# Kernel tuning notes

Measured on AMD Instinct MI355X. Metric: run time of the kernel, lower is better.

The kernel has to match this reference:

```python
import jax, jax.numpy as jnp
import numpy as np
import math

B, H, N, L = 8, 512, 64, 2048


def setup_inputs() -> dict:
    key = jax.random.key(0)
    k_u, k_c, k_dt, k_d, k_w, k_b, k_ar, k_ai = jax.random.split(key, 8)
    u = jax.random.normal(k_u, (B, H, L), dtype=jnp.float32)
    # C ~ complex randn, stored as (..., 2) real/imag pairs (torch.view_as_real)
    C_ri = jax.random.normal(k_c, (H, N, 2), dtype=jnp.float32)
    # log_dt ~ Uniform(log(dt_min), log(dt_max))
    lo, hi = math.log(0.001), math.log(0.1)
    log_dt = jax.random.uniform(k_dt, (H,), dtype=jnp.float32) * (hi - lo) + lo
    D = jax.random.normal(k_d, (H,), dtype=jnp.float32)
    # Conv1d(H, 2H, kernel_size=1) -> weight (2H, H), bias (2H), kaiming-ish scale
    W = jax.random.normal(k_w, (2 * H, H), dtype=jnp.float32) / math.sqrt(H)
    b = jax.random.normal(k_b, (2 * H,), dtype=jnp.float32) * 0.01
    # Fixed diagonal state matrix A: Re(A) uniform in [-0.9, -0.8), Im(A) random
    a_re = -0.9 + 0.1 * jax.random.uniform(k_ar, (N,), dtype=jnp.float32)
    a_im = math.pi * jnp.arange(N, dtype=jnp.float32)  # stable oscillation freqs
    A_ri = jnp.stack([a_re, a_im], axis=-1)
    return {"u": u, "C_ri": C_ri, "log_dt": log_dt, "D": D, "W": W, "b": b, "A_ri": A_ri}


def _forward(u, C_ri, log_dt, D, W, b, A_ri):
    Lseq = u.shape[-1]
    C = C_ri[..., 0] + 1j * C_ri[..., 1]          # (H, N) complex
    A = A_ri[..., 0] + 1j * A_ri[..., 1]          # (N,) complex
    dt = jnp.exp(log_dt)                           # (H,)
    dtA = dt[:, None] * A[None, :]                 # (H, N)
    # Vandermonde: exp(dtA * l) for l in [0, L)  -> (H, N, L) complex
    K = jnp.exp(dtA[:, :, None] * jnp.arange(Lseq, dtype=jnp.float32))
    Ct = C * (jnp.exp(dtA) - 1.0) / A              # (H, N)
    k = 2.0 * jnp.einsum('hn,hnl->hl', Ct, K).real  # (H, L) real kernel
    # FFT long convolution (linear conv via length-2L circular conv)
    nfft = 2 * Lseq
    y = jnp.fft.irfft(jnp.fft.rfft(u, n=nfft) * jnp.fft.rfft(k, n=nfft), n=nfft)[..., :Lseq]
    y = y + D[:, None] * u                         # skip connection
    y = jax.nn.gelu(y, approximate=False)          # torch nn.GELU default = exact erf
    # Conv1d kernel_size=1 == per-position linear, then GLU over channel dim
    z = jnp.einsum('oh,bhl->bol', W, y) + b[:, None]  # (B, 2H, L)
    a, g = jnp.split(z, 2, axis=-2)
    return a * jax.nn.sigmoid(g)                   # (B, H, L)


def reference(u, C_ri, log_dt, D, W, b, A_ri):
    return _forward(u, C_ri, log_dt, D, W, b, A_ri)
```

## Files before the change

kernel.cpp:

```cpp
#include <hip/hip_runtime.h>
#include <math.h>

#define Hh 512
#define Nn 64
#define Ll 2048
#define Bb 8

typedef float f32x4 __attribute__((ext_vector_type(4)));
typedef __bf16 bf16x8 __attribute__((ext_vector_type(8)));

__device__ __forceinline__ unsigned short f2b(float x) {
  unsigned u = __builtin_bit_cast(unsigned, x);
  u += 0x7FFFu + ((u >> 16) & 1u);
  return (unsigned short)(u >> 16);
}
__device__ __forceinline__ float b2f(unsigned short b) {
  unsigned u = ((unsigned)b) << 16;
  return __builtin_bit_cast(float, u);
}

union BF8 {
  unsigned short us[8];
  bf16x8 v;
  uint4 q;
};

__device__ __forceinline__ uint4 cvt8q(const float* p) {
  float4 a = *(const float4*)p;
  float4 b = *(const float4*)(p + 4);
  BF8 o;
  o.us[0] = f2b(a.x); o.us[1] = f2b(a.y); o.us[2] = f2b(a.z); o.us[3] = f2b(a.w);
  o.us[4] = f2b(b.x); o.us[5] = f2b(b.y); o.us[6] = f2b(b.z); o.us[7] = f2b(b.w);
  return o.q;
}

__device__ __forceinline__ float gelu_f(float y) {
  float t = y * y;
  float p = y * fmaf(0.0713548162726f, t, 1.59576912161f);
  float e = __expf(-p);
  return y / (1.0f + e);
}

__global__ __launch_bounds__(256) void prep_kernel(
    const float* __restrict__ C_ri, const float* __restrict__ log_dt,
    const float* __restrict__ A_ri, unsigned short* __restrict__ A1,
    unsigned short* __restrict__ A2, float* __restrict__ lamQ) {
  __shared__ char sm[49152];
  __shared__ float kqs[64];
  __shared__ float kpart[4][64];
  float* kt = (float*)sm;
  char* A1s = sm;
  char* A2s = sm + 16384;
  int h = blockIdx.x;
  int tid = threadIdx.x, n = tid & 63, part = tid >> 6;

  float dt = expf(log_dt[h]);
  float ar = A_ri[2 * n], ai = A_ri[2 * n + 1];
  float er = expf(dt * ar);
  float sn, cs;
  sincosf(dt * ai, &sn, &cs);
  float lr = er * cs, li = er * sn;
  float em1r = lr - 1.0f, em1i = li;
  float cr = C_ri[(h * 64 + n) * 2], ci = C_ri[(h * 64 + n) * 2 + 1];
  float numr = cr * em1r - ci * em1i;
  float numi = cr * em1i + ci * em1r;
  float den = ar * ar + ai * ai;
  float ctr = (numr * ar + numi * ai) / den;
  float cti = (numi * ar - numr * ai) / den;
  float l16r = lr, l16i = li;
#pragma unroll
  for (int s = 0; s < 4; ++s) {
    float t = l16r * l16r - l16i * l16i;
    l16i = 2.0f * l16r * l16i;
    l16r = t;
  }
  if (part == 0) {
    float qr = l16r, qi = l16i;
#pragma unroll
    for (int s = 0; s < 2; ++s) {
      float t = qr * qr - qi * qi;
      qi = 2.0f * qr * qi;
      qr = t;
    }
    lamQ[h * 128 + 2 * n] = qr;
    lamQ[h * 128 + 2 * n + 1] = qi;
  }
  float lpr = 1.0f, lpi = 0.0f;
  for (int s = 0; s < part; ++s) {
    float t = lpr * l16r - lpi * l16i;
    lpi = lpr * l16i + lpi * l16r;
    lpr = t;
  }
  int e0 = part * 16;
  {
    float vr = ctr * lpr - cti * lpi, vi = ctr * lpi + cti * lpr;
#pragma unroll
    for (int j = 0; j < 16; ++j) {
      kt[(e0 + j) * 64 + n] = vr;
      float t = vr * lr - vi * li;
      vi = vr * li + vi * lr;
      vr = t;
    }
  }
  __syncthreads();
  {
    float s = 0.0f;
#pragma unroll
    for (int j = 0; j < 16; ++j) s += kt[n * 64 + ((e0 + j + n) & 63)];
    kpart[part][n] = s;
  }
  __syncthreads();
  if (part == 0) kqs[n] = 2.0f * (kpart[0][n] + kpart[1][n] + kpart[2][n] + kpart[3][n]);
  __syncthreads();
  {
    BF8 R0, R1, I0, I1;
    float vr = lpr, vi = lpi;
#pragma unroll
    for (int j = 0; j < 16; ++j) {
      int idx = 15 - j;
      if (idx < 8) { R0.us[idx] = f2b(vr); I0.us[idx] = f2b(vi); }
      else         { R1.us[idx - 8] = f2b(vr); I1.us[idx - 8] = f2b(vi); }
      float t = vr * lr - vi * li;
      vi = vr * li + vi * lr;
      vr = t;
    }
    int qlo = 48 - e0;
    int rowR = 2 * n, rowI = 2 * n + 1;
    *(uint4*)(A1s + ((rowR * 128 + 2 * qlo) ^ ((rowR & 7) << 4))) = R0.q;
    *(uint4*)(A1s + ((rowR * 128 + 2 * qlo + 16) ^ ((rowR & 7) << 4))) = R1.q;
    *(uint4*)(A1s + ((rowI * 128 + 2 * qlo) ^ ((rowI & 7) << 4))) = I0.q;
    *(uint4*)(A1s + ((rowI * 128 + 2 * qlo + 16) ^ ((rowI & 7) << 4))) = I1.q;
  }
  {
    float c1r = ctr * lr - cti * li, c1i = ctr * li + cti * lr;
    float wr = 2.0f * (c1r * lpr - c1i * lpi);
    float wi = 2.0f * (c1r * lpi + c1i * lpr);
#pragma unroll
    for (int j = 0; j < 16; ++j) {
      int t = e0 + j;
      *(unsigned*)(A2s + ((t * 512 + 128 + 4 * n) ^ ((t & 7) << 4))) =
          (unsigned)f2b(wr) | ((unsigned)f2b(-wi) << 16);
      float tm = wr * lr - wi * li;
      wi = wr * li + wi * lr;
      wr = tm;
    }
  }
  {
    int tau = n;
#pragma unroll
    for (int half = 0; half < 2; ++half) {
      int q0 = e0 + half * 8;
      BF8 o;
#pragma unroll
      for (int j = 0; j < 8; ++j) {
        int q = q0 + j;
        o.us[j] = (q <= tau) ? f2b(kqs[tau - q]) : (unsigned short)0;
      }
      *(uint4*)(A2s + ((tau * 512 + 2 * q0) ^ ((tau & 7) << 4))) = o.q;
    }
  }
  __syncthreads();
#pragma unroll
  for (int i = 0; i < 4; ++i) {
    int byte = (i * 256 + tid) * 16;
    int row = byte >> 7;
    *(uint4*)((char*)A1 + (size_t)h * 16384 + byte) =
        *(const uint4*)(A1s + (byte ^ ((row & 7) << 4)));
  }
#pragma unroll
  for (int i = 0; i < 8; ++i) {
    int idx = i * 256 + tid;
    int row = idx >> 5;
    int byte = row * 512 + (idx & 31) * 16;
    *(uint4*)((char*)A2 + (size_t)h * 32768 + byte) =
        *(const uint4*)(A2s + (byte ^ ((row & 7) << 4)));
  }
}

__global__ __launch_bounds__(256) void wcvt_kernel(const float* __restrict__ W,
                                                   unsigned short* __restrict__ Wimg) {
  int id = blockIdx.x * 256 + threadIdx.x;
  int slot = id & 3, row = (id >> 2) & 127, kt = (id >> 9) & 15, ot = id >> 13;
  int o = (row < 64) ? (ot * 64 + row) : (512 + ot * 64 + row - 64);
  uint4 v = cvt8q(W + (size_t)o * 512 + kt * 32 + slot * 8);
  int sp = slot ^ ((row >> 1) & 3);
  *(uint4*)((char*)Wimg + (((size_t)ot * 16 + kt) * 8192) + row * 64 + sp * 16) = v;
}

__global__ __launch_bounds__(256, 5) void fused_conv_kernel(
    const float* __restrict__ u, const unsigned short* __restrict__ A1,
    const unsigned short* __restrict__ A2, const float* __restrict__ lamQ,
    const float* __restrict__ Dv, unsigned short* __restrict__ gy) {
  __shared__ char SXb[16384];
  __shared__ char Ub[8192];
  __shared__ float2 sX16[2][64];
  int h = blockIdx.x;
  int bs = blockIdx.y * 2;
  int tid = threadIdx.x;
  int w = tid >> 6, lane = tid & 63, lg = lane >> 4, l15 = lane & 15;

  {
    int row = tid >> 2, k0 = (tid & 3) * 16;
    int b = bs + (row >> 5), c = row & 31;
    const float* up = u + ((size_t)(b * Hh + h)) * Ll + c * 64 + k0;
    uint4 v0 = cvt8q(up), v1 = cvt8q(up + 8);
    int base = row * 128 + k0 * 2;
    int swz = (row & 7) << 4;
    *(uint4*)(Ub + (base ^ swz)) = v0;
    *(uint4*)(Ub + ((base + 16) ^ swz)) = v1;
  }
  bf16x8 a1f[2][2];
#pragma unroll
  for (int i = 0; i < 2; ++i) {
    int row = (2 * w + i) * 16 + l15;
#pragma unroll
    for (int kb = 0; kb < 2; ++kb)
      a1f[i][kb] = *(const bf16x8*)(A1 + ((size_t)h * 128 + row) * 64 + kb * 32 + lg * 8);
  }
  __syncthreads();

#pragma unroll
  for (int ct = 0; ct < 4; ++ct) {
    int bc = ct * 16 + l15;
    bf16x8 bu[2];
#pragma unroll
    for (int kb = 0; kb < 2; ++kb)
      bu[kb] = *(const bf16x8*)(Ub + ((bc * 128 + kb * 64 + lg * 16) ^ ((bc & 7) << 4)));
#pragma unroll
    for (int i = 0; i < 2; ++i) {
      f32x4 acc = {0.f, 0.f, 0.f, 0.f};
      acc = __builtin_amdgcn_mfma_f32_16x16x32_bf16(a1f[i][0], bu[0], acc, 0, 0, 0);
      acc = __builtin_amdgcn_mfma_f32_16x16x32_bf16(a1f[i][1], bu[1], acc, 0, 0, 0);
      int n2q = (2 * w + i) * 16 + lg * 4;
      uint2 pk;
      pk.x = f2b(acc[0]) | ((unsigned)f2b(acc[1]) << 16);
      pk.y = f2b(acc[2]) | ((unsigned)f2b(acc[3]) << 16);
      *(uint2*)(SXb + ((bc * 256 + n2q * 2) ^ ((bc & 7) << 4))) = pk;
    }
  }
  __syncthreads();

  bf16x8 a2f[6];
  int rowA = w * 16 + l15;
#pragma unroll
  for (int kb = 0; kb < 6; ++kb)
    a2f[kb] = *(const bf16x8*)(A2 + ((size_t)h * 64 + rowA) * 256 + kb * 32 + lg * 8);

  int nn = tid & 63, bpart = tid >> 6;
  int rbloc = bpart >> 1, rhalf = bpart & 1;
  float lqr = lamQ[h * 128 + 2 * nn], lqi = lamQ[h * 128 + 2 * nn + 1];
  {
    float Xr = 0.f, Xi = 0.f;
    int cbase = rbloc * 32 + rhalf * 16;
    for (int c = 0; c < 16; ++c) {
      int bc = cbase + c;
      int byte = (bc * 256 + 4 * nn) ^ ((bc & 7) << 4);
      unsigned ps = *(const unsigned*)(SXb + byte);
      *(unsigned*)(SXb + byte) = (unsigned)f2b(Xr) | ((unsigned)f2b(Xi) << 16);
      float Sr = b2f((unsigned short)(ps & 0xFFFF));
      float Si = b2f((unsigned short)(ps >> 16));
      float nXr = lqr * Xr - lqi * Xi + Sr;
      float nXi = lqr * Xi + lqi * Xr + Si;
      Xr = nXr;
      Xi = nXi;
    }
    if (rhalf == 0) sX16[rbloc][nn] = make_float2(Xr, Xi);
  }
  __syncthreads();
  if (rhalf) {
    float2 x16 = sX16[rbloc][nn];
    float cr = x16.x, ci = x16.y;
    int cbase = rbloc * 32 + 16;
#pragma unroll
    for (int c = 0; c < 16; ++c) {
      int bc = cbase + c;
      int byte = (bc * 256 + 4 * nn) ^ ((bc & 7) << 4);
      unsigned pv = *(const unsigned*)(SXb + byte);
      float vr = b2f((unsigned short)(pv & 0xFFFF)) + cr;
      float vi = b2f((unsigned short)(pv >> 16)) + ci;
      *(unsigned*)(SXb + byte) = (unsigned)f2b(vr) | ((unsigned)f2b(vi) << 16);
      float t = cr * lqr - ci * lqi;
      ci = cr * lqi + ci * lqr;
      cr = t;
    }
  }
  __syncthreads();

  float Dh = Dv[h];
  int t0 = w * 16 + lg * 4;
  f32x4 acc4[4];
  uint2 usk[4];
#pragma unroll
  for (int ct = 0; ct < 4; ++ct) {
    int bc = ct * 16 + l15;
    f32x4 acc = {0.f, 0.f, 0.f, 0.f};
#pragma unroll
    for (int kb = 0; kb < 2; ++kb) {
      bf16x8 bu = *(const bf16x8*)(Ub + ((bc * 128 + kb * 64 + lg * 16) ^ ((bc & 7) << 4)));
      acc = __builtin_amdgcn_mfma_f32_16x16x32_bf16(a2f[kb], bu, acc, 0, 0, 0);
    }
#pragma unroll
    for (int kb = 2; kb < 6; ++kb) {
      bf16x8 bx = *(const bf16x8*)(SXb + ((bc * 256 + ((kb - 2) * 32 + lg * 8) * 2) ^ ((bc & 7) << 4)));
      acc = __builtin_amdgcn_mfma_f32_16x16x32_bf16(a2f[kb], bx, acc, 0, 0, 0);
    }
    acc4[ct] = acc;
    usk[ct] = *(const uint2*)(Ub + ((bc * 128 + t0 * 2) ^ ((bc & 7) << 4)));
  }
  __syncthreads();

#pragma unroll
  for (int ct = 0; ct < 4; ++ct) {
    int bc = ct * 16 + l15;
    const unsigned short* up = (const unsigned short*)&usk[ct];
    unsigned short e[4];
#pragma unroll
    for (int r = 0; r < 4; ++r) {
      float y = fmaf(Dh, b2f(up[r]), acc4[ct][r]);
      e[r] = f2b(gelu_f(y));
    }
    uint2 pk;
    pk.x = e[0] | ((unsigned)e[1] << 16);
    pk.y = e[2] | ((unsigned)e[3] << 16);
    *(uint2*)(Ub + ((bc * 128 + t0 * 2) ^ ((bc & 7) << 4))) = pk;
  }
  __syncthreads();

#pragma unroll
  for (int i = 0; i < 2; ++i) {
    int j = tid + 256 * i;
    int row = j >> 3, q = j & 7;
    int byte = row * 128 + q * 16;
    uint4 v = *(const uint4*)(Ub + (byte ^ ((row & 7) << 4)));
    int b = bs + (row >> 5), c = row & 31;
    *(uint4*)(gy + ((size_t)(b * Hh + h)) * Ll + c * 64 + q * 8) = v;
  }
}

__global__ __launch_bounds__(256, 3) void glu_kernel(
    const unsigned short* __restrict__ Wimg, const unsigned short* __restrict__ gy,
    const float* __restrict__ bias, float* __restrict__ out) {
  __shared__ char sA[2][8192];
  __shared__ char sB[2][8192];
  int lt = blockIdx.x;
  int ot = blockIdx.y;
  int b = lt >> 4, lseg = lt & 15;
  int t = threadIdx.x;
  int lane = t & 63, lg = lane >> 4, l15 = lane & 15;
  int w = t >> 6, wm = w >> 1, wn = w & 1;
  int p = t >> 4, cg = t & 15;
  const char* Abase = (const char*)Wimg + (size_t)ot * 131072;
  const unsigned short* gybase = gy + (size_t)b * Hh * Ll + lseg * 128 + cg * 8 + 2 * p * Ll;

  int offA[2], offG[2];
#pragma unroll
  for (int mt = 0; mt < 2; ++mt) {
    int rA = wm * 32 + mt * 16 + l15;
    offA[mt] = rA * 64 + ((lg ^ ((rA >> 1) & 3)) << 4);
    int rG = rA + 64;
    offG[mt] = rG * 64 + ((lg ^ ((rG >> 1) & 3)) << 4);
  }
  int offB[4];
#pragma unroll
  for (int nt = 0; nt < 4; ++nt) {
    int rB = wn * 64 + nt * 16 + l15;
    int pr = ((rB >> 3) << 3) | ((rB & 7) ^ ((rB >> 3) & 7));
    offB[nt] = (lg << 11) + (pr << 4);
  }
  int offW[8];
#pragma unroll
  for (int j = 0; j < 8; ++j) {
    int pr = (cg << 3) | (j ^ (cg & 7));
    offW[j] = ((p >> 2) << 11) + (pr << 4) + ((p & 3) << 2);
  }

  f32x4 accA[2][4], accG[2][4];
#pragma unroll
  for (int mt = 0; mt < 2; ++mt)
#pragma unroll
    for (int nt = 0; nt < 4; ++nt) {
      accA[mt][nt] = (f32x4){0.f, 0.f, 0.f, 0.f};
      accG[mt][nt] = (f32x4){0.f, 0.f, 0.f, 0.f};
    }

  {
    const char* ga = Abase + t * 16;
    __builtin_amdgcn_global_load_lds(ga, (char*)&sA[0][0] + t * 16, 16, 0, 0);
    __builtin_amdgcn_global_load_lds(ga + 4096, (char*)&sA[0][0] + 4096 + t * 16, 16, 0, 0);
    BF8 r0, r1;
    r0.q = *(const uint4*)gybase;
    r1.q = *(const uint4*)(gybase + Ll);
#pragma unroll
    for (int j = 0; j < 8; ++j)
      *(unsigned*)(&sB[0][0] + offW[j]) =
          (unsigned)r0.us[j] | ((unsigned)r1.us[j] << 16);
  }
  __syncthreads();

  for (int kt = 0; kt < 16; ++kt) {
    int cur = kt & 1;
    BF8 r0, r1;
    if (kt < 15) {
      const char* ga = Abase + (kt + 1) * 8192 + t * 16;
      char* da = (char*)&sA[cur ^ 1][0] + t * 16;
      __builtin_amdgcn_global_load_lds(ga, da, 16, 0, 0);
      __builtin_amdgcn_global_load_lds(ga + 4096, da + 4096, 16, 0, 0);
      r0.q = *(const uint4*)(gybase + (size_t)(kt + 1) * 32 * Ll);
      r1.q = *(const uint4*)(gybase + (size_t)(kt + 1) * 32 * Ll + Ll);
    }
    const char* bufA = &sA[cur][0];
    const char* bufB = &sB[cur][0];
    bf16x8 aA[2], aG[2], bB[4];
#pragma unroll
    for (int mt = 0; mt < 2; ++mt) {
      aA[mt] = *(const bf16x8*)(bufA + offA[mt]);
      aG[mt] = *(const bf16x8*)(bufA + offG[mt]);
    }
#pragma unroll
    for (int nt = 0; nt < 4; ++nt)
      bB[nt] = *(const bf16x8*)(bufB + offB[nt]);
#pragma unroll
    for (int mt = 0; mt < 2; ++mt)
#pragma unroll
      for (int nt = 0; nt < 4; ++nt) {
        accA[mt][nt] = __builtin_amdgcn_mfma_f32_16x16x32_bf16(bB[nt], aA[mt], accA[mt][nt], 0, 0, 0);
        accG[mt][nt] = __builtin_amdgcn_mfma_f32_16x16x32_bf16(bB[nt], aG[mt], accG[mt][nt], 0, 0, 0);
      }
    if (kt < 15) {
      char* db = &sB[cur ^ 1][0];
#pragma unroll
      for (int j = 0; j < 8; ++j)
        *(unsigned*)(db + offW[j]) =
            (unsigned)r0.us[j] | ((unsigned)r1.us[j] << 16);
    }
    __syncthreads();
  }

#pragma unroll
  for (int mt = 0; mt < 2; ++mt) {
    int oA = ot * 64 + wm * 32 + mt * 16 + l15;
    float ba = bias[oA];
    float bg = bias[512 + oA];
    float* orow = out + ((size_t)(b * Hh) + oA) * Ll + lseg * 128 + wn * 64 + lg * 4;
#pragma unroll
    for (int nt = 0; nt < 4; ++nt) {
      float4 res;
      float* rp = (float*)&res;
#pragma unroll
      for (int r = 0; r < 4; ++r) {
        float a = accA[mt][nt][r] + ba;
        float g = accG[mt][nt][r] + bg;
        rp[r] = a * (1.0f / (1.0f + __expf(-g)));
      }
      *(float4*)(orow + nt * 16) = res;
    }
  }
}

extern "C" void kernel_launch(void* const* d_in, const int* in_sizes, int n_in,
                              void* d_out, int out_size, void* d_ws,
                              size_t ws_size, hipStream_t stream) {
  const float* u      = (const float*)d_in[0];
  const float* C_ri   = (const float*)d_in[1];
  const float* log_dt = (const float*)d_in[2];
  const float* Dv     = (const float*)d_in[3];
  const float* W      = (const float*)d_in[4];
  const float* bias   = (const float*)d_in[5];
  const float* A_ri   = (const float*)d_in[6];
  float* out = (float*)d_out;

  char* ws = (char*)d_ws;
  unsigned short* A1   = (unsigned short*)ws;
  unsigned short* A2   = (unsigned short*)(ws + 8388608);
  float*          lamQ = (float*)(ws + 25165824);
  unsigned short* Wimg = (unsigned short*)(ws + 25427968);
  unsigned short* gy   = (unsigned short*)(ws + 26476544);

  prep_kernel<<<Hh, 256, 0, stream>>>(C_ri, log_dt, A_ri, A1, A2, lamQ);
  wcvt_kernel<<<256, 256, 0, stream>>>(W, Wimg);
  fused_conv_kernel<<<dim3(Hh, 4), 256, 0, stream>>>(u, A1, A2, lamQ, Dv, gy);
  glu_kernel<<<dim3(128, 8), 256, 0, stream>>>(Wimg, gy, bias, out);
}
```

Measured before the change: 62.74 us.

## Pre-transpose GLU activations into swizzled tile image for direct LDS loads

Adds a transpose kernel that rewrites the bf16 activations gy into a pre-swizzled, K-interleaved tile image (reusing the A1 workspace region). The GLU GEMM can then stream B tiles with async global_load_lds, as it already does for the W tiles, instead of staging them through registers with per-element repacking and LDS stores. Occupancy is raised to 4 blocks per CU. The cost is an extra kernel launch and a full extra read and write of the 16 MB activation tensor.

```diff
diff --git a/kernel.cpp b/kernel.cpp
--- a/kernel.cpp
+++ b/kernel.cpp
@@ -337,8 +337,43 @@
   }
 }
 
-__global__ __launch_bounds__(256, 3) void glu_kernel(
-    const unsigned short* __restrict__ Wimg, const unsigned short* __restrict__ gy,
+__global__ __launch_bounds__(256) void transpose_kernel(
+    const unsigned short* __restrict__ gy, unsigned short* __restrict__ Bimg) {
+  __shared__ char Sl[8192];
+  int ktb = blockIdx.x, lseg = blockIdx.y, b = blockIdx.z;
+  int t = threadIdx.x;
+  int h0 = ktb * 32, l0 = lseg * 128;
+  {
+    int h = t >> 3, seg = t & 7;
+    const unsigned short* g = gy + ((size_t)(b * Hh) + h0 + h) * Ll + l0 + seg * 16;
+    uint4 v0 = *(const uint4*)g;
+    uint4 v1 = *(const uint4*)(g + 8);
+    int sw = (h & 7) << 4;
+    *(uint4*)(Sl + h * 256 + ((seg * 32) ^ sw)) = v0;
+    *(uint4*)(Sl + h * 256 + ((seg * 32 + 16) ^ sw)) = v1;
+  }
+  __syncthreads();
+  {
+    int l = t >> 1, q = t & 1;
+    unsigned w[8];
+#pragma unroll
+    for (int i = 0; i < 8; ++i) {
+      int p = q * 8 + i;
+      int hA = 2 * p, hB = 2 * p + 1;
+      unsigned short u0 = *(const unsigned short*)(Sl + hA * 256 + ((2 * l) ^ ((hA & 7) << 4)));
+      unsigned short u1 = *(const unsigned short*)(Sl + hB * 256 + ((2 * l) ^ ((hB & 7) << 4)));
+      w[i] = (unsigned)u0 | ((unsigned)u1 << 16);
+    }
+    size_t tb = (((size_t)(b * 16 + lseg)) * 16 + ktb) * 8192 + l * 64;
+    int swl = (l >> 1) & 3;
+    int sp0 = (2 * q) ^ swl, sp1 = (2 * q + 1) ^ swl;
+    *(uint4*)((char*)Bimg + tb + sp0 * 16) = *(uint4*)&w[0];
+    *(uint4*)((char*)Bimg + tb + sp1 * 16) = *(uint4*)&w[4];
+  }
+}
+
+__global__ __launch_bounds__(256, 4) void glu_kernel(
+    const unsigned short* __restrict__ Wimg, const unsigned short* __restrict__ Bimg,
     const float* __restrict__ bias, float* __restrict__ out) {
   __shared__ char sA[2][8192];
   __shared__ char sB[2][8192];
@@ -348,11 +383,10 @@
   int t = threadIdx.x;
   int lane = t & 63, lg = lane >> 4, l15 = lane & 15;
   int w = t >> 6, wm = w >> 1, wn = w & 1;
-  int p = t >> 4, cg = t & 15;
   const char* Abase = (const char*)Wimg + (size_t)ot * 131072;
-  const unsigned short* gybase = gy + (size_t)b * Hh * Ll + lseg * 128 + cg * 8 + 2 * p * Ll;
-
-  int offA[2], offG[2];
+  const char* Bbase = (const char*)Bimg + ((size_t)b * 16 + lseg) * 131072;
+
+  int offA[2], offG[2], offB[4];
 #pragma unroll
   for (int mt = 0; mt < 2; ++mt) {
     int rA = wm * 32 + mt * 16 + l15;
@@ -360,18 +394,10 @@
     int rG = rA + 64;
     offG[mt] = rG * 64 + ((lg ^ ((rG >> 1) & 3)) << 4);
   }
-  int offB[4];
 #pragma unroll
   for (int nt = 0; nt < 4; ++nt) {
     int rB = wn * 64 + nt * 16 + l15;
-    int pr = ((rB >> 3) << 3) | ((rB & 7) ^ ((rB >> 3) & 7));
-    offB[nt] = (lg << 11) + (pr << 4);
-  }
-  int offW[8];
-#pragma unroll
-  for (int j = 0; j < 8; ++j) {
-    int pr = (cg << 3) | (j ^ (cg & 7));
-    offW[j] = ((p >> 2) << 11) + (pr << 4) + ((p & 3) << 2);
+    offB[nt] = rB * 64 + ((lg ^ ((rB >> 1) & 3)) << 4);
   }
 
   f32x4 accA[2][4], accG[2][4];
@@ -385,28 +411,25 @@
 
   {
     const char* ga = Abase + t * 16;
+    const char* gb = Bbase + t * 16;
     __builtin_amdgcn_global_load_lds(ga, (char*)&sA[0][0] + t * 16, 16, 0, 0);
     __builtin_amdgcn_global_load_lds(ga + 4096, (char*)&sA[0][0] + 4096 + t * 16, 16, 0, 0);
-    BF8 r0, r1;
-    r0.q = *(const uint4*)gybase;
-    r1.q = *(const uint4*)(gybase + Ll);
-#pragma unroll
-    for (int j = 0; j < 8; ++j)
-      *(unsigned*)(&sB[0][0] + offW[j]) =
-          (unsigned)r0.us[j] | ((unsigned)r1.us[j] << 16);
+    __builtin_amdgcn_global_load_lds(gb, (char*)&sB[0][0] + t * 16, 16, 0, 0);
+    __builtin_amdgcn_global_load_lds(gb + 4096, (char*)&sB[0][0] + 4096 + t * 16, 16, 0, 0);
   }
   __syncthreads();
 
   for (int kt = 0; kt < 16; ++kt) {
     int cur = kt & 1;
-    BF8 r0, r1;
     if (kt < 15) {
       const char* ga = Abase + (kt + 1) * 8192 + t * 16;
+      const char* gb = Bbase + (kt + 1) * 8192 + t * 16;
       char* da = (char*)&sA[cur ^ 1][0] + t * 16;
+      char* db = (char*)&sB[cur ^ 1][0] + t * 16;
       __builtin_amdgcn_global_load_lds(ga, da, 16, 0, 0);
       __builtin_amdgcn_global_load_lds(ga + 4096, da + 4096, 16, 0, 0);
-      r0.q = *(const uint4*)(gybase + (size_t)(kt + 1) * 32 * Ll);
-      r1.q = *(const uint4*)(gybase + (size_t)(kt + 1) * 32 * Ll + Ll);
+      __builtin_amdgcn_global_load_lds(gb, db, 16, 0, 0);
+      __builtin_amdgcn_global_load_lds(gb + 4096, db + 4096, 16, 0, 0);
     }
     const char* bufA = &sA[cur][0];
     const char* bufB = &sB[cur][0];
@@ -426,13 +449,6 @@
         accA[mt][nt] = __builtin_amdgcn_mfma_f32_16x16x32_bf16(bB[nt], aA[mt], accA[mt][nt], 0, 0, 0);
         accG[mt][nt] = __builtin_amdgcn_mfma_f32_16x16x32_bf16(bB[nt], aG[mt], accG[mt][nt], 0, 0, 0);
       }
-    if (kt < 15) {
-      char* db = &sB[cur ^ 1][0];
-#pragma unroll
-      for (int j = 0; j < 8; ++j)
-        *(unsigned*)(db + offW[j]) =
-            (unsigned)r0.us[j] | ((unsigned)r1.us[j] << 16);
-    }
     __syncthreads();
   }
 
@@ -475,9 +491,11 @@
   float*          lamQ = (float*)(ws + 25165824);
   unsigned short* Wimg = (unsigned short*)(ws + 25427968);
   unsigned short* gy   = (unsigned short*)(ws + 26476544);
+  unsigned short* Bimg = (unsigned short*)ws;
 
   prep_kernel<<<Hh, 256, 0, stream>>>(C_ri, log_dt, A_ri, A1, A2, lamQ);
   wcvt_kernel<<<256, 256, 0, stream>>>(W, Wimg);
   fused_conv_kernel<<<dim3(Hh, 4), 256, 0, stream>>>(u, A1, A2, lamQ, Dv, gy);
-  glu_kernel<<<dim3(128, 8), 256, 0, stream>>>(Wimg, gy, bias, out);
-}
+  transpose_kernel<<<dim3(16, 16, Bb), 256, 0, stream>>>(gy, Bimg);
+  glu_kernel<<<dim3(128, 8), 256, 0, stream>>>(Wimg, Bimg, bias, out);
+}
```

New measurement: 72.56 us. 15.6% more time.
